# Performance work log

Hardware: AMD Instinct MI355X
Metric: run time of the kernel (lower is better)

The kernel has to match this reference:

```python
import jax, jax.numpy as jnp
import numpy as np

TEMP = 0.5   # temperature from __init__
EPS = 1e-8   # torch.nn.CosineSimilarity eps


def setup_inputs() -> dict:
    key = jax.random.key(0)
    N, D = 8192, 256
    x = jax.random.normal(key, (N, D), dtype=jnp.float32)
    # pairs: each label appears exactly twice, as required for the
    # sim[~mask].reshape(N, -1) in the original to be well-formed
    y = jnp.arange(N, dtype=jnp.int32) // 2
    return {"x": x, "y": y}


def reference(x, y):
    # cosine similarity matrix: normalize once, then one NxD @ DxN matmul
    # (equivalent to CosineSimilarity(x.unsqueeze(1), x.unsqueeze(0)) without
    #  the NxNxD intermediate)
    norm = jnp.maximum(jnp.linalg.norm(x, axis=1, keepdims=True), EPS)
    xn = x / norm
    sim = (xn @ xn.T) / TEMP                     # [N, N]

    # Original: positives = equal-label entries (row-major order, includes the
    # diagonal), logits = [positives | negatives] which is just a per-row
    # permutation of sim; labels = 0 -> CE target is the FIRST equal-label
    # column of each row. logsumexp is over the full row (all N entries).
    eq = y[:, None] == y[None, :]                # [N, N] bool
    first_pos = jnp.argmax(eq, axis=1)           # first column j with y_j == y_i
    target = jnp.take_along_axis(sim, first_pos[:, None], axis=1)[:, 0]  # [N]

    lse = jax.nn.logsumexp(sim, axis=1)          # [N]
    N = x.shape[0]
    loss = jnp.sum(lse - target) / N             # CrossEntropyLoss(sum) / N
    return loss
```

## Files before the change

kernel.cpp:

```cpp
#include <hip/hip_runtime.h>
#include <hip/hip_bf16.h>

#define D 256
#define INV_TEMP 2.0f

typedef __attribute__((ext_vector_type(8))) short short8;
typedef __attribute__((ext_vector_type(4))) float floatx4;
typedef __attribute__((ext_vector_type(4))) unsigned short ushortx4;

__device__ __forceinline__ unsigned short f2bf(float f) {
    union { float f; unsigned u; } a; a.f = f;
    unsigned r = (a.u + 0x7fffu + ((a.u >> 16) & 1u)) >> 16;
    return (unsigned short)r;
}

__device__ __forceinline__ void gload_lds16(const unsigned short* g,
                                            unsigned short* l) {
    __builtin_amdgcn_global_load_lds(
        (const __attribute__((address_space(1))) unsigned int*)g,
        (__attribute__((address_space(3))) unsigned int*)l, 16, 0, 0);
}

__global__ void nt_prep_kernel(const float* __restrict__ x,
                               unsigned short* __restrict__ xnb,
                               float* __restrict__ pair_dot,
                               float* __restrict__ rowsum,
                               float* __restrict__ gsum,
                               unsigned int* __restrict__ gcnt) {
    if (blockIdx.x == 0 && threadIdx.x == 0) { *gsum = 0.f; *gcnt = 0u; }
    if (blockIdx.x < 32) rowsum[blockIdx.x * 256 + threadIdx.x] = 0.f;
    int p    = blockIdx.x * 4 + (threadIdx.x >> 6);
    int lane = threadIdx.x & 63;
    const float4* a4 = (const float4*)(x + (size_t)(2 * p) * D);
    const float4* b4 = (const float4*)(x + (size_t)(2 * p + 1) * D);
    float4 a = a4[lane], b = b4[lane];
    float saa = a.x * a.x + a.y * a.y + a.z * a.z + a.w * a.w;
    float sbb = b.x * b.x + b.y * b.y + b.z * b.z + b.w * b.w;
    float sab = a.x * b.x + a.y * b.y + a.z * b.z + a.w * b.w;
    #pragma unroll
    for (int off = 32; off; off >>= 1) {
        saa += __shfl_xor(saa, off);
        sbb += __shfl_xor(sbb, off);
        sab += __shfl_xor(sab, off);
    }
    float inva = 1.0f / fmaxf(sqrtf(saa), 1e-8f);
    float invb = 1.0f / fmaxf(sqrtf(sbb), 1e-8f);
    ushortx4 oa, ob;
    oa.x = f2bf(a.x * inva); oa.y = f2bf(a.y * inva);
    oa.z = f2bf(a.z * inva); oa.w = f2bf(a.w * inva);
    ob.x = f2bf(b.x * invb); ob.y = f2bf(b.y * invb);
    ob.z = f2bf(b.z * invb); ob.w = f2bf(b.w * invb);
    __builtin_nontemporal_store(oa, (ushortx4*)(xnb + (size_t)(2 * p) * D) + lane);
    __builtin_nontemporal_store(ob, (ushortx4*)(xnb + (size_t)(2 * p + 1) * D) + lane);
    if (lane == 0)
        pair_dot[p] = sab * inva * invb * INV_TEMP;
}

__global__ __launch_bounds__(512, 2)
void nt_simexp_kernel(const unsigned short* __restrict__ xnb,
                      float* __restrict__ rowsum) {
    __shared__ __align__(16) unsigned short As[4][256 * 32];
    __shared__ __align__(16) unsigned short Bs[4][256 * 32];

    int b = (int)blockIdx.x;
    b = (b & 7) * 66 + (b >> 3);
    int ti = (int)((sqrtf(8.f * (float)b + 1.f) - 1.f) * 0.5f);
    while ((ti + 1) * (ti + 2) / 2 <= b) ++ti;
    while (ti * (ti + 1) / 2 > b) --ti;
    const int tj = b - ti * (ti + 1) / 2;

    const int tid  = threadIdx.x;
    const int wave = tid >> 6, lane = tid & 63;
    const int wm   = wave >> 2, wn = wave & 3;
    const int quad = lane >> 4, c = lane & 15;
    const int pA   = quad ^ ((c >> 1) & 3);

    const unsigned short* Abase = xnb + (size_t)ti * 256 * D;
    const unsigned short* Bbase = xnb + (size_t)tj * 256 * D;

    auto stage = [&](int kst, int buf) {
        const int rl = lane >> 2, pq = lane & 3;
        #pragma unroll
        for (int t = 0; t < 2; ++t) {
            int wl = wave * 2 + t;
            int rr = wl * 16 + rl;
            int j  = pq ^ ((rr >> 1) & 3);
            gload_lds16(Abase + (size_t)rr * D + kst * 32 + j * 8,
                        As[buf] + wl * 512 + lane * 8);
        }
        #pragma unroll
        for (int t = 0; t < 2; ++t) {
            int wl = wave * 2 + t;
            int rr = wl * 16 + rl;
            int j  = pq ^ ((rr >> 1) & 3);
            gload_lds16(Bbase + (size_t)rr * D + kst * 32 + j * 8,
                        Bs[buf] + wl * 512 + lane * 8);
        }
    };

    stage(0, 0); stage(1, 1); stage(2, 2);

    floatx4 acc[8][4];
    #pragma unroll
    for (int mt = 0; mt < 8; ++mt)
        #pragma unroll
        for (int nt = 0; nt < 4; ++nt)
            acc[mt][nt] = (floatx4){0.f, 0.f, 0.f, 0.f};

    #pragma unroll
    for (int t = 0; t < 8; ++t) {
        asm volatile("s_waitcnt vmcnt(8)" ::: "memory");
        __builtin_amdgcn_s_barrier();
        asm volatile("" ::: "memory");

        const int buf = t & 3;
        short8 af[8], bf[4];
        #pragma unroll
        for (int mt = 0; mt < 8; ++mt)
            af[mt] = *(const short8*)(As[buf] + (wm * 8 + mt) * 512 +
                                      (c * 4 + pA) * 8);
        #pragma unroll
        for (int nt = 0; nt < 4; ++nt)
            bf[nt] = *(const short8*)(Bs[buf] + (wn * 4 + nt) * 512 +
                                      (c * 4 + pA) * 8);

        if (t < 7) stage((t + 3) & 7, (t + 3) & 3);

        __builtin_amdgcn_s_setprio(1);
        #pragma unroll
        for (int mt = 0; mt < 8; ++mt)
            #pragma unroll
            for (int nt = 0; nt < 4; ++nt)
                acc[mt][nt] = __builtin_amdgcn_mfma_f32_16x16x32_bf16(
                    af[mt], bf[nt], acc[mt][nt], 0, 0, 0);
        __builtin_amdgcn_s_setprio(0);
    }

    #pragma unroll
    for (int mt = 0; mt < 8; ++mt)
        #pragma unroll
        for (int nt = 0; nt < 4; ++nt)
            #pragma unroll
            for (int r = 0; r < 4; ++r)
                acc[mt][nt][r] = __expf(acc[mt][nt][r] * INV_TEMP);

    #pragma unroll
    for (int mt = 0; mt < 8; ++mt) {
        float ps[4] = {0.f, 0.f, 0.f, 0.f};
        #pragma unroll
        for (int nt = 0; nt < 4; ++nt)
            #pragma unroll
            for (int r = 0; r < 4; ++r)
                ps[r] += acc[mt][nt][r];
        #pragma unroll
        for (int off = 1; off < 16; off <<= 1)
            #pragma unroll
            for (int r = 0; r < 4; ++r)
                ps[r] += __shfl_xor(ps[r], off);
        if (c < 4) {
            float v = (c == 0) ? ps[0] : (c == 1) ? ps[1]
                    : (c == 2) ? ps[2] : ps[3];
            atomicAdd(&rowsum[ti * 256 + wm * 128 + mt * 16 + quad * 4 + c], v);
        }
    }
    if (ti != tj) {
        #pragma unroll
        for (int nt = 0; nt < 4; ++nt) {
            float cs = 0.f;
            #pragma unroll
            for (int mt = 0; mt < 8; ++mt)
                #pragma unroll
                for (int r = 0; r < 4; ++r)
                    cs += acc[mt][nt][r];
            cs += __shfl_xor(cs, 16);
            cs += __shfl_xor(cs, 32);
            if (quad == 0)
                atomicAdd(&rowsum[tj * 256 + wn * 64 + nt * 16 + c], cs);
        }
    }
}

__global__ void nt_reduce_kernel(const float* __restrict__ rowsum,
                                 const float* __restrict__ pair_dot,
                                 float* __restrict__ gsum,
                                 unsigned int* __restrict__ gcnt,
                                 float* __restrict__ out, int N) {
    __shared__ float sm[8];
    int r = blockIdx.x * 512 + threadIdx.x;
    float v = logf(rowsum[r]);
    if (r & 1) v -= pair_dot[r >> 1];
    #pragma unroll
    for (int off = 32; off; off >>= 1) v += __shfl_xor(v, off);
    int lane = threadIdx.x & 63, wv = threadIdx.x >> 6;
    if (lane == 0) sm[wv] = v;
    __syncthreads();
    if (threadIdx.x == 0) {
        float s = sm[0] + sm[1] + sm[2] + sm[3]
                + sm[4] + sm[5] + sm[6] + sm[7];
        atomicAdd(gsum, s);
        __threadfence();
        if (atomicAdd(gcnt, 1u) == 15u) {
            __threadfence();
            float t = atomicAdd(gsum, 0.0f);
            out[0] = (t - (float)N) / (float)N;
        }
    }
}

extern "C" void kernel_launch(void* const* d_in, const int* in_sizes, int n_in,
                              void* d_out, int out_size, void* d_ws, size_t ws_size,
                              hipStream_t stream) {
    const float* x = (const float*)d_in[0];
    int N = in_sizes[0] / D;

    char* ws = (char*)d_ws;
    unsigned short* xnb = (unsigned short*)ws;
    float* pair_dot  = (float*)(ws + (size_t)N * D * 2);
    float* rowsum    = pair_dot + N / 2;
    float* gsum      = rowsum + N;
    unsigned int* gcnt = (unsigned int*)(gsum + 1);

    nt_prep_kernel<<<N / 8, 256, 0, stream>>>(x, xnb, pair_dot, rowsum,
                                              gsum, gcnt);
    nt_simexp_kernel<<<528, 512, 0, stream>>>(xnb, rowsum);
    nt_reduce_kernel<<<16, 512, 0, stream>>>(rowsum, pair_dot, gsum, gcnt,
                                             (float*)d_out, N);
}
```

Before: 99.67 us.

## Switch to persistent 256x128 triangular tiles with balanced per-block work lists

Replaces the 528-block grid of 256x256 triangle tiles with 512 blocks of 256 threads. Each block processes two or three 256x128 tiles chosen by a pairing scheme meant to balance the triangular work, and prefetches continuously across tile boundaries through a three-slot LDS ring. The goal is to remove the tail imbalance of 528 blocks over the available CUs and to keep loads flowing between tiles. In exchange, each block does more serial work with fewer waves, and the smaller tiles raise operand reload traffic and the number of atomics.

```diff
diff --git a/kernel.cpp b/kernel.cpp
--- a/kernel.cpp
+++ b/kernel.cpp
@@ -56,126 +56,138 @@
         pair_dot[p] = sab * inva * invb * INV_TEMP;
 }
 
-__global__ __launch_bounds__(512, 2)
+__global__ __launch_bounds__(256, 2)
 void nt_simexp_kernel(const unsigned short* __restrict__ xnb,
                       float* __restrict__ rowsum) {
-    __shared__ __align__(16) unsigned short As[4][256 * 32];
-    __shared__ __align__(16) unsigned short Bs[4][256 * 32];
-
-    int b = (int)blockIdx.x;
-    b = (b & 7) * 66 + (b >> 3);
-    int ti = (int)((sqrtf(8.f * (float)b + 1.f) - 1.f) * 0.5f);
-    while ((ti + 1) * (ti + 2) / 2 <= b) ++ti;
-    while (ti * (ti + 1) / 2 > b) --ti;
-    const int tj = b - ti * (ti + 1) / 2;
-
-    const int tid  = threadIdx.x;
-    const int wave = tid >> 6, lane = tid & 63;
-    const int wm   = wave >> 2, wn = wave & 3;
+    __shared__ __align__(16) unsigned short As[3][256 * 32];
+    __shared__ __align__(16) unsigned short Bs[3][128 * 32];
+
+    const int p  = blockIdx.x & 31, q = blockIdx.x >> 5;
+    const int s1 = 63 - p;
+    const int cnt0 = 32 - (p >> 1);
+    const int q0 = (p + q) & 15;
+    const int ntiles = (q0 == 0) ? 3 : 2;
+
+    const int wave = threadIdx.x >> 6, lane = threadIdx.x & 63;
+    const int wm = wave >> 1, wn = wave & 1;
     const int quad = lane >> 4, c = lane & 15;
-    const int pA   = quad ^ ((c >> 1) & 3);
-
-    const unsigned short* Abase = xnb + (size_t)ti * 256 * D;
-    const unsigned short* Bbase = xnb + (size_t)tj * 256 * D;
-
-    auto stage = [&](int kst, int buf) {
+    const int pA = quad ^ ((c >> 1) & 3);
+
+    auto j_of = [&](int m) { return (m < cnt0) ? p : s1; };
+    auto i_of = [&](int m) { return (m < cnt0) ? (p >> 1) + m
+                                               : (s1 >> 1) + (m - cnt0); };
+
+    auto stage_g = [&](int g) {
+        int k = g >> 3;
+        if (k >= ntiles) k = ntiles - 1;
+        const int ph = g & 7, slot = g % 3;
+        const int i = i_of(q0 + 16 * k), j = j_of(q0 + 16 * k);
         const int rl = lane >> 2, pq = lane & 3;
+        const unsigned short* asrc = xnb + (size_t)(i * 256) * D + ph * 32;
+        #pragma unroll
+        for (int t = 0; t < 4; ++t) {
+            int wl = wave * 4 + t;
+            int rr = wl * 16 + rl;
+            int jj = pq ^ ((rr >> 1) & 3);
+            gload_lds16(asrc + (size_t)rr * D + jj * 8,
+                        As[slot] + wl * 512 + lane * 8);
+        }
+        const unsigned short* bsrc = xnb + (size_t)(j * 128) * D + ph * 32;
         #pragma unroll
         for (int t = 0; t < 2; ++t) {
             int wl = wave * 2 + t;
             int rr = wl * 16 + rl;
-            int j  = pq ^ ((rr >> 1) & 3);
-            gload_lds16(Abase + (size_t)rr * D + kst * 32 + j * 8,
-                        As[buf] + wl * 512 + lane * 8);
-        }
-        #pragma unroll
-        for (int t = 0; t < 2; ++t) {
-            int wl = wave * 2 + t;
-            int rr = wl * 16 + rl;
-            int j  = pq ^ ((rr >> 1) & 3);
-            gload_lds16(Bbase + (size_t)rr * D + kst * 32 + j * 8,
-                        Bs[buf] + wl * 512 + lane * 8);
+            int jj = pq ^ ((rr >> 1) & 3);
+            gload_lds16(bsrc + (size_t)rr * D + jj * 8,
+                        Bs[slot] + wl * 512 + lane * 8);
         }
     };
 
-    stage(0, 0); stage(1, 1); stage(2, 2);
+    stage_g(0); stage_g(1);
 
     floatx4 acc[8][4];
-    #pragma unroll
-    for (int mt = 0; mt < 8; ++mt)
-        #pragma unroll
-        for (int nt = 0; nt < 4; ++nt)
-            acc[mt][nt] = (floatx4){0.f, 0.f, 0.f, 0.f};
-
-    #pragma unroll
-    for (int t = 0; t < 8; ++t) {
-        asm volatile("s_waitcnt vmcnt(8)" ::: "memory");
-        __builtin_amdgcn_s_barrier();
-        asm volatile("" ::: "memory");
-
-        const int buf = t & 3;
-        short8 af[8], bf[4];
+
+    for (int k = 0; k < ntiles; ++k) {
+        const int m = q0 + 16 * k;
+        const int i = i_of(m), j = j_of(m);
+
         #pragma unroll
         for (int mt = 0; mt < 8; ++mt)
-            af[mt] = *(const short8*)(As[buf] + (wm * 8 + mt) * 512 +
-                                      (c * 4 + pA) * 8);
-        #pragma unroll
-        for (int nt = 0; nt < 4; ++nt)
-            bf[nt] = *(const short8*)(Bs[buf] + (wn * 4 + nt) * 512 +
-                                      (c * 4 + pA) * 8);
-
-        if (t < 7) stage((t + 3) & 7, (t + 3) & 3);
-
-        __builtin_amdgcn_s_setprio(1);
+            #pragma unroll
+            for (int nt = 0; nt < 4; ++nt)
+                acc[mt][nt] = (floatx4){0.f, 0.f, 0.f, 0.f};
+
+        #pragma unroll
+        for (int s = 0; s < 8; ++s) {
+            const int g = k * 8 + s;
+            asm volatile("s_waitcnt vmcnt(6)" ::: "memory");
+            __builtin_amdgcn_s_barrier();
+            asm volatile("" ::: "memory");
+
+            const int slot = g % 3;
+            short8 af[8], bf[4];
+            #pragma unroll
+            for (int mt = 0; mt < 8; ++mt)
+                af[mt] = *(const short8*)(As[slot] + (wm * 8 + mt) * 512 +
+                                          (c * 4 + pA) * 8);
+            #pragma unroll
+            for (int nt = 0; nt < 4; ++nt)
+                bf[nt] = *(const short8*)(Bs[slot] + (wn * 4 + nt) * 512 +
+                                          (c * 4 + pA) * 8);
+
+            stage_g(g + 2);
+
+            __builtin_amdgcn_s_setprio(1);
+            #pragma unroll
+            for (int mt = 0; mt < 8; ++mt)
+                #pragma unroll
+                for (int nt = 0; nt < 4; ++nt)
+                    acc[mt][nt] = __builtin_amdgcn_mfma_f32_16x16x32_bf16(
+                        af[mt], bf[nt], acc[mt][nt], 0, 0, 0);
+            __builtin_amdgcn_s_setprio(0);
+        }
+
         #pragma unroll
         for (int mt = 0; mt < 8; ++mt)
             #pragma unroll
             for (int nt = 0; nt < 4; ++nt)
-                acc[mt][nt] = __builtin_amdgcn_mfma_f32_16x16x32_bf16(
-                    af[mt], bf[nt], acc[mt][nt], 0, 0, 0);
-        __builtin_amdgcn_s_setprio(0);
-    }
-
-    #pragma unroll
-    for (int mt = 0; mt < 8; ++mt)
-        #pragma unroll
-        for (int nt = 0; nt < 4; ++nt)
-            #pragma unroll
-            for (int r = 0; r < 4; ++r)
-                acc[mt][nt][r] = __expf(acc[mt][nt][r] * INV_TEMP);
-
-    #pragma unroll
-    for (int mt = 0; mt < 8; ++mt) {
-        float ps[4] = {0.f, 0.f, 0.f, 0.f};
-        #pragma unroll
-        for (int nt = 0; nt < 4; ++nt)
-            #pragma unroll
-            for (int r = 0; r < 4; ++r)
-                ps[r] += acc[mt][nt][r];
-        #pragma unroll
-        for (int off = 1; off < 16; off <<= 1)
-            #pragma unroll
-            for (int r = 0; r < 4; ++r)
-                ps[r] += __shfl_xor(ps[r], off);
-        if (c < 4) {
-            float v = (c == 0) ? ps[0] : (c == 1) ? ps[1]
-                    : (c == 2) ? ps[2] : ps[3];
-            atomicAdd(&rowsum[ti * 256 + wm * 128 + mt * 16 + quad * 4 + c], v);
-        }
-    }
-    if (ti != tj) {
-        #pragma unroll
-        for (int nt = 0; nt < 4; ++nt) {
-            float cs = 0.f;
-            #pragma unroll
-            for (int mt = 0; mt < 8; ++mt)
                 #pragma unroll
                 for (int r = 0; r < 4; ++r)
-                    cs += acc[mt][nt][r];
-            cs += __shfl_xor(cs, 16);
-            cs += __shfl_xor(cs, 32);
-            if (quad == 0)
-                atomicAdd(&rowsum[tj * 256 + wn * 64 + nt * 16 + c], cs);
+                    acc[mt][nt][r] = __expf(acc[mt][nt][r] * INV_TEMP);
+
+        #pragma unroll
+        for (int mt = 0; mt < 8; ++mt) {
+            float ps[4] = {0.f, 0.f, 0.f, 0.f};
+            #pragma unroll
+            for (int nt = 0; nt < 4; ++nt)
+                #pragma unroll
+                for (int r = 0; r < 4; ++r)
+                    ps[r] += acc[mt][nt][r];
+            #pragma unroll
+            for (int off = 1; off < 16; off <<= 1)
+                #pragma unroll
+                for (int r = 0; r < 4; ++r)
+                    ps[r] += __shfl_xor(ps[r], off);
+            if (c < 4) {
+                float v = (c == 0) ? ps[0] : (c == 1) ? ps[1]
+                        : (c == 2) ? ps[2] : ps[3];
+                atomicAdd(&rowsum[i * 256 + wm * 128 + mt * 16 + quad * 4 + c], v);
+            }
+        }
+        if ((j >> 1) < i) {
+            #pragma unroll
+            for (int nt = 0; nt < 4; ++nt) {
+                float cs = 0.f;
+                #pragma unroll
+                for (int mt = 0; mt < 8; ++mt)
+                    #pragma unroll
+                    for (int r = 0; r < 4; ++r)
+                        cs += acc[mt][nt][r];
+                cs += __shfl_xor(cs, 16);
+                cs += __shfl_xor(cs, 32);
+                if (quad == 0)
+                    atomicAdd(&rowsum[j * 128 + wn * 64 + nt * 16 + c], cs);
+            }
         }
     }
 }
@@ -222,7 +234,7 @@
 
     nt_prep_kernel<<<N / 8, 256, 0, stream>>>(x, xnb, pair_dot, rowsum,
                                               gsum, gcnt);
-    nt_simexp_kernel<<<528, 512, 0, stream>>>(xnb, rowsum);
+    nt_simexp_kernel<<<512, 256, 0, stream>>>(xnb, rowsum);
     nt_reduce_kernel<<<16, 512, 0, stream>>>(rowsum, pair_dot, gsum, gcnt,
                                              (float*)d_out, N);
 }
```

New measurement: 160.6 us. 1.61x slower.
